# Kernel tuning notes

Measured on AMD Instinct MI355X. Metric: run time of the kernel, lower is better.

The kernel has to match this reference:

```python
import jax, jax.numpy as jnp
import numpy as np


def setup_inputs() -> dict:
    key = jax.random.key(0)
    k1, k2 = jax.random.split(key)
    B, S, D, L = 4, 4096, 256, 8921
    x = jax.random.normal(k1, (B, S, D), dtype=jnp.float32)
    U = jax.random.normal(k2, (L, D), dtype=jnp.float32)
    return {"x": x, "U": U}


def reference(x, U):
    # scores: [B, L, S] = U [L,D] @ x^T [B,D,S]
    scores = jnp.einsum('ld,bsd->bls', U, x)
    # softmax over seq dim (dim=2 in torch)
    alpha = jax.nn.softmax(scores, axis=2)
    # pooled: [B, L, D]
    out = jnp.einsum('bls,bsd->bld', alpha, x)
    return (out, alpha)
```

## Files before the change

kernel.cpp:

```cpp
#include <hip/hip_runtime.h>

#define B_DIM 4
#define S_DIM 4096
#define D_DIM 256
#define L_DIM 8921
#define L_PAD 8960

typedef _Float16 f16x8 __attribute__((ext_vector_type(8)));
typedef _Float16 f16x4 __attribute__((ext_vector_type(4)));
typedef float    f32x4 __attribute__((ext_vector_type(4)));

__device__ __forceinline__ void cp16(_Float16* lds, const _Float16* g) {
  __builtin_amdgcn_global_load_lds(
      (const __attribute__((address_space(1))) unsigned int*)g,
      (__attribute__((address_space(3))) unsigned int*)lds, 16, 0, 0);
}

__global__ __launch_bounds__(256) void k_split_x(const float* __restrict__ x,
                                                 _Float16* __restrict__ xh,
                                                 _Float16* __restrict__ xl) {
  const size_t i = ((size_t)blockIdx.x * 256 + threadIdx.x) * 4;
  float4 v = *(const float4*)(x + i);
  f16x4 h, l;
  h.x = (_Float16)v.x; l.x = (_Float16)(v.x - (float)h.x);
  h.y = (_Float16)v.y; l.y = (_Float16)(v.y - (float)h.y);
  h.z = (_Float16)v.z; l.z = (_Float16)(v.z - (float)h.z);
  h.w = (_Float16)v.w; l.w = (_Float16)(v.w - (float)h.w);
  *(f16x4*)(xh + i) = h;
  *(f16x4*)(xl + i) = l;
}

__global__ __launch_bounds__(256) void k_split_u(const float* __restrict__ U,
                                                 _Float16* __restrict__ uh,
                                                 _Float16* __restrict__ ul) {
  const size_t i = ((size_t)blockIdx.x * 256 + threadIdx.x) * 4;
  if (i >= (size_t)L_PAD * D_DIM) return;
  float4 v = make_float4(0.f, 0.f, 0.f, 0.f);
  if (i < (size_t)L_DIM * D_DIM) v = *(const float4*)(U + i);
  f16x4 h, l;
  h.x = (_Float16)v.x; l.x = (_Float16)(v.x - (float)h.x);
  h.y = (_Float16)v.y; l.y = (_Float16)(v.y - (float)h.y);
  h.z = (_Float16)v.z; l.z = (_Float16)(v.z - (float)h.z);
  h.w = (_Float16)v.w; l.w = (_Float16)(v.w - (float)h.w);
  *(f16x4*)(uh + i) = h;
  *(f16x4*)(ul + i) = l;
}

__global__ __launch_bounds__(256) void k_transpose(const float* __restrict__ x,
                                                   _Float16* __restrict__ xT) {
  __shared__ _Float16 t[32][33];
  const int s0 = blockIdx.x * 32, d0 = blockIdx.y * 32, b = blockIdx.z;
  const float* xb = x + (size_t)b * S_DIM * D_DIM;
  const int r = threadIdx.x >> 5, c = threadIdx.x & 31;
#pragma unroll
  for (int p = 0; p < 4; ++p) {
    const int row = r + p * 8;
    t[row][c] = (_Float16)xb[(size_t)(s0 + row) * D_DIM + d0 + c];
  }
  __syncthreads();
  _Float16* xtb = xT + (size_t)b * D_DIM * S_DIM;
#pragma unroll
  for (int p = 0; p < 4; ++p) {
    const int row = r + p * 8;
    xtb[(size_t)(d0 + row) * S_DIM + s0 + c] = t[c][row];
  }
}

__global__ __launch_bounds__(256) void k_scores(const _Float16* __restrict__ Uh,
                                                const _Float16* __restrict__ Ul,
                                                const _Float16* __restrict__ Xh,
                                                const _Float16* __restrict__ Xl,
                                                float* __restrict__ scores,
                                                float2* __restrict__ part) {
  const int s0 = blockIdx.x * 128;
  const int l0 = blockIdx.y * 128;
  const int b  = blockIdx.z;

  __shared__ __attribute__((aligned(16))) _Float16 Ah[128 * 32];
  __shared__ __attribute__((aligned(16))) _Float16 Al[128 * 32];
  __shared__ __attribute__((aligned(16))) _Float16 Bh[128 * 32];
  __shared__ __attribute__((aligned(16))) _Float16 Bl[128 * 32];

  const int tid = threadIdx.x;
  const int wave = tid >> 6, lane = tid & 63;
  const int wm = wave & 1, wn = wave >> 1;

  const _Float16* Xbh = Xh + (size_t)b * S_DIM * D_DIM;
  const _Float16* Xbl = Xl + (size_t)b * S_DIM * D_DIM;

  const int srow = tid >> 2;
  const int csrc = ((tid & 3) ^ ((tid >> 3) & 3)) * 8;
  const size_t urow0 = (size_t)(l0 + srow) * D_DIM + csrc;
  const size_t urow1 = urow0 + (size_t)64 * D_DIM;
  const size_t xrow0 = (size_t)(s0 + srow) * D_DIM + csrc;
  const size_t xrow1 = xrow0 + (size_t)64 * D_DIM;
  _Float16* d0 = (_Float16*)0 + tid * 8;
  const int ldso = tid * 8;

  const int frow = lane & 15;
  const int ck = ((lane >> 4) ^ ((frow >> 1) & 3)) * 8;

  f32x4 acc[4][4] = {};

  for (int k0 = 0; k0 < D_DIM; k0 += 32) {
    cp16(Ah + ldso,        Uh + urow0 + k0);
    cp16(Ah + 2048 + ldso, Uh + urow1 + k0);
    cp16(Al + ldso,        Ul + urow0 + k0);
    cp16(Al + 2048 + ldso, Ul + urow1 + k0);
    cp16(Bh + ldso,        Xbh + xrow0 + k0);
    cp16(Bh + 2048 + ldso, Xbh + xrow1 + k0);
    cp16(Bl + ldso,        Xbl + xrow0 + k0);
    cp16(Bl + 2048 + ldso, Xbl + xrow1 + k0);
    __syncthreads();

    f16x8 ah[4], al[4], bh[4], bl[4];
#pragma unroll
    for (int i = 0; i < 4; ++i) {
      const int ra = (wm * 64 + i * 16 + frow) * 32 + ck;
      const int rb = (wn * 64 + i * 16 + frow) * 32 + ck;
      ah[i] = *(const f16x8*)(Ah + ra);
      al[i] = *(const f16x8*)(Al + ra);
      bh[i] = *(const f16x8*)(Bh + rb);
      bl[i] = *(const f16x8*)(Bl + rb);
    }
#pragma unroll
    for (int i = 0; i < 4; ++i)
#pragma unroll
      for (int j = 0; j < 4; ++j) {
        acc[i][j] = __builtin_amdgcn_mfma_f32_16x16x32_f16(ah[i], bh[j], acc[i][j], 0, 0, 0);
        acc[i][j] = __builtin_amdgcn_mfma_f32_16x16x32_f16(ah[i], bl[j], acc[i][j], 0, 0, 0);
        acc[i][j] = __builtin_amdgcn_mfma_f32_16x16x32_f16(al[i], bh[j], acc[i][j], 0, 0, 0);
      }
    __syncthreads();
  }
  (void)d0;

  float* sc = scores + (size_t)b * L_DIM * S_DIM;
  const int hi = lane >> 4;
#pragma unroll
  for (int i = 0; i < 4; ++i)
#pragma unroll
    for (int j = 0; j < 4; ++j) {
      const int col = s0 + wn * 64 + j * 16 + (lane & 15);
#pragma unroll
      for (int r = 0; r < 4; ++r) {
        const int row = l0 + wm * 64 + i * 16 + hi * 4 + r;
        if (row < L_DIM) sc[(size_t)row * S_DIM + col] = acc[i][j][r];
      }
    }

  float* redm = (float*)Ah;
  float* reds = redm + 256;
#pragma unroll
  for (int i = 0; i < 4; ++i)
#pragma unroll
    for (int r = 0; r < 4; ++r) {
      float m = fmaxf(fmaxf(acc[i][0][r], acc[i][1][r]),
                      fmaxf(acc[i][2][r], acc[i][3][r]));
      m = fmaxf(m, __shfl_xor(m, 1));
      m = fmaxf(m, __shfl_xor(m, 2));
      m = fmaxf(m, __shfl_xor(m, 4));
      m = fmaxf(m, __shfl_xor(m, 8));
      float s = __expf(acc[i][0][r] - m) + __expf(acc[i][1][r] - m) +
                __expf(acc[i][2][r] - m) + __expf(acc[i][3][r] - m);
      s += __shfl_xor(s, 1);
      s += __shfl_xor(s, 2);
      s += __shfl_xor(s, 4);
      s += __shfl_xor(s, 8);
      if ((lane & 15) == 0) {
        const int row64 = i * 16 + hi * 4 + r;
        redm[(wm * 2 + wn) * 64 + row64] = m;
        reds[(wm * 2 + wn) * 64 + row64] = s;
      }
    }
  __syncthreads();
  if (tid < 128) {
    const int wmm = tid >> 6, r64 = tid & 63;
    const float m0 = redm[(wmm * 2 + 0) * 64 + r64];
    const float m1 = redm[(wmm * 2 + 1) * 64 + r64];
    const float s0v = reds[(wmm * 2 + 0) * 64 + r64];
    const float s1v = reds[(wmm * 2 + 1) * 64 + r64];
    const float m = fmaxf(m0, m1);
    const float s = s0v * __expf(m0 - m) + s1v * __expf(m1 - m);
    const int l = l0 + tid;
    if (l < L_DIM)
      part[((size_t)blockIdx.x * B_DIM + b) * L_PAD + l] = make_float2(m, s);
  }
}

__global__ __launch_bounds__(256) void k_sreduce(const float2* __restrict__ part,
                                                 float* __restrict__ stats) {
  const int idx = blockIdx.x * 256 + threadIdx.x;
  if (idx >= B_DIM * L_DIM) return;
  const int b = idx / L_DIM;
  const int l = idx - b * L_DIM;
  float2 v[32];
#pragma unroll
  for (int t = 0; t < 32; ++t) v[t] = part[((size_t)t * B_DIM + b) * L_PAD + l];
  float m = v[0].x;
#pragma unroll
  for (int t = 1; t < 32; ++t) m = fmaxf(m, v[t].x);
  float s = 0.f;
#pragma unroll
  for (int t = 0; t < 32; ++t) s += v[t].y * __expf(v[t].x - m);
  stats[2 * (size_t)idx]     = m;
  stats[2 * (size_t)idx + 1] = 1.0f / s;
}

__global__ __launch_bounds__(256) void k_out(const _Float16* __restrict__ XT,
                                             const float* __restrict__ stats,
                                             float* __restrict__ alpha,
                                             float* __restrict__ out) {
  const int l0 = blockIdx.x * 32;
  const int b  = blockIdx.y;
  const int tid = threadIdx.x;
  const int wave = tid >> 6, lane = tid & 63;

  __shared__ __attribute__((aligned(16))) _Float16 Aa[32 * 40];
  __shared__ __attribute__((aligned(16))) _Float16 Bb[256 * 40];
  __shared__ float sm[32], sr[32];

  if (tid < 32) {
    const int l = l0 + tid;
    float m = 0.f, r = 0.f;
    if (l < L_DIM) {
      const float* st = stats + ((size_t)b * L_DIM + l) * 2;
      m = st[0];
      r = st[1];
    }
    sm[tid] = m;
    sr[tid] = r;
  }
  __syncthreads();

  f32x4 acc[2][4] = {};
  float* al_base = alpha + (size_t)b * L_DIM * S_DIM;
  const _Float16* xt = XT + (size_t)b * D_DIM * S_DIM;

  const int arow = tid >> 3, aoff = (tid & 7) * 4;
  const int brow = tid >> 2, boff = (tid & 3) * 8;
  const float m_r = sm[arow], r_r = sr[arow];
  const int l_a = l0 + arow;
  const int frow = lane & 15, fk = (lane >> 4) * 8;

  for (int s0 = 0; s0 < S_DIM; s0 += 32) {
    float4 v = make_float4(0.f, 0.f, 0.f, 0.f);
    if (l_a < L_DIM) {
      float* ap = al_base + (size_t)l_a * S_DIM + s0 + aoff;
      v = *(const float4*)ap;
      v.x = __expf(v.x - m_r) * r_r;
      v.y = __expf(v.y - m_r) * r_r;
      v.z = __expf(v.z - m_r) * r_r;
      v.w = __expf(v.w - m_r) * r_r;
      *(float4*)ap = v;
    }
    f16x4 pk;
    pk.x = (_Float16)v.x;
    pk.y = (_Float16)v.y;
    pk.z = (_Float16)v.z;
    pk.w = (_Float16)v.w;
    *(f16x4*)(Aa + arow * 40 + aoff) = pk;
#pragma unroll
    for (int p = 0; p < 4; ++p) {
      const int row = brow + p * 64;
      *(uint4*)(Bb + row * 40 + boff) =
          *(const uint4*)(xt + (size_t)row * S_DIM + s0 + boff);
    }
    __syncthreads();

    f16x8 af[2], bf[4];
    af[0] = *(const f16x8*)(Aa + frow * 40 + fk);
    af[1] = *(const f16x8*)(Aa + (16 + frow) * 40 + fk);
#pragma unroll
    for (int j = 0; j < 4; ++j)
      bf[j] = *(const f16x8*)(Bb + (wave * 64 + j * 16 + frow) * 40 + fk);
#pragma unroll
    for (int i = 0; i < 2; ++i)
#pragma unroll
      for (int j = 0; j < 4; ++j)
        acc[i][j] = __builtin_amdgcn_mfma_f32_16x16x32_f16(af[i], bf[j], acc[i][j], 0, 0, 0);
    __syncthreads();
  }

  float* ob = out + (size_t)b * L_DIM * D_DIM;
#pragma unroll
  for (int i = 0; i < 2; ++i)
#pragma unroll
    for (int j = 0; j < 4; ++j) {
      const int d = wave * 64 + j * 16 + (lane & 15);
#pragma unroll
      for (int r = 0; r < 4; ++r) {
        const int l = l0 + i * 16 + (lane >> 4) * 4 + r;
        if (l < L_DIM) ob[(size_t)l * D_DIM + d] = acc[i][j][r];
      }
    }
}

extern "C" void kernel_launch(void* const* d_in, const int* in_sizes, int n_in,
                              void* d_out, int out_size, void* d_ws, size_t ws_size,
                              hipStream_t stream) {
  const float* x = (const float*)d_in[0];
  const float* U = (const float*)d_in[1];
  float* out   = (float*)d_out;
  float* alpha = out + (size_t)B_DIM * L_DIM * D_DIM;

  const size_t NX  = (size_t)B_DIM * S_DIM * D_DIM;
  const size_t NUP = (size_t)L_PAD * D_DIM;

  char* w = (char*)d_ws;
  _Float16* xh = (_Float16*)w; w += NX * 2;
  _Float16* xl = (_Float16*)w; w += NX * 2;
  _Float16* xT = (_Float16*)w; w += NX * 2;
  _Float16* uh = (_Float16*)w; w += NUP * 2;
  _Float16* ul = (_Float16*)w; w += NUP * 2;
  float* stats = (float*)w;    w += (size_t)B_DIM * L_DIM * 2 * sizeof(float);
  float2* part = (float2*)w;

  k_split_x<<<dim3((unsigned)(NX / 1024)), 256, 0, stream>>>(x, xh, xl);
  k_split_u<<<dim3((unsigned)(NUP / 1024)), 256, 0, stream>>>(U, uh, ul);
  k_transpose<<<dim3(S_DIM / 32, D_DIM / 32, B_DIM), 256, 0, stream>>>(x, xT);
  k_scores<<<dim3(S_DIM / 128, L_PAD / 128, B_DIM), 256, 0, stream>>>(
      uh, ul, xh, xl, alpha, part);
  k_sreduce<<<dim3((B_DIM * L_DIM + 255) / 256), 256, 0, stream>>>(part, stats);
  k_out<<<dim3((L_DIM + 31) / 32, B_DIM), 256, 0, stream>>>(xT, stats, alpha, out);
}
```

Before: 1.323 ms.

## Double-buffer k_out tiles with async LDS loads and prefetch of alpha

Rewrites the k_out main loop to double-buffer the A (softmax probabilities) and B (transposed x) tiles in LDS. The next X^T tile is issued via global_load_lds and the next alpha vector is prefetched into registers while the current tile's MFMAs run, and the trailing barrier is dropped. It also replaces the padded LDS layout with an XOR-swizzled one. The aim is to hide global load latency and cut one barrier per iteration, at the cost of doubled LDS use and a more delicate ordering of barriers around the buffers.

```diff
diff --git a/kernel.cpp b/kernel.cpp
--- a/kernel.cpp
+++ b/kernel.cpp
@@ -94,7 +94,6 @@
   const size_t urow1 = urow0 + (size_t)64 * D_DIM;
   const size_t xrow0 = (size_t)(s0 + srow) * D_DIM + csrc;
   const size_t xrow1 = xrow0 + (size_t)64 * D_DIM;
-  _Float16* d0 = (_Float16*)0 + tid * 8;
   const int ldso = tid * 8;
 
   const int frow = lane & 15;
@@ -133,7 +132,6 @@
       }
     __syncthreads();
   }
-  (void)d0;
 
   float* sc = scores + (size_t)b * L_DIM * S_DIM;
   const int hi = lane >> 4;
@@ -216,8 +214,8 @@
   const int tid = threadIdx.x;
   const int wave = tid >> 6, lane = tid & 63;
 
-  __shared__ __attribute__((aligned(16))) _Float16 Aa[32 * 40];
-  __shared__ __attribute__((aligned(16))) _Float16 Bb[256 * 40];
+  __shared__ __attribute__((aligned(16))) _Float16 Aa[2][32 * 32];
+  __shared__ __attribute__((aligned(16))) _Float16 Bb[2][256 * 32];
   __shared__ float sm[32], sr[32];
 
   if (tid < 32) {
@@ -237,49 +235,64 @@
   float* al_base = alpha + (size_t)b * L_DIM * S_DIM;
   const _Float16* xt = XT + (size_t)b * D_DIM * S_DIM;
 
-  const int arow = tid >> 3, aoff = (tid & 7) * 4;
-  const int brow = tid >> 2, boff = (tid & 3) * 8;
+  const int arow = tid >> 3, a8 = tid & 7;
+  const int aoff = a8 * 4;
   const float m_r = sm[arow], r_r = sr[arow];
   const int l_a = l0 + arow;
-  const int frow = lane & 15, fk = (lane >> 4) * 8;
-
-  for (int s0 = 0; s0 < S_DIM; s0 += 32) {
-    float4 v = make_float4(0.f, 0.f, 0.f, 0.f);
-    if (l_a < L_DIM) {
-      float* ap = al_base + (size_t)l_a * S_DIM + s0 + aoff;
-      v = *(const float4*)ap;
-      v.x = __expf(v.x - m_r) * r_r;
-      v.y = __expf(v.y - m_r) * r_r;
-      v.z = __expf(v.z - m_r) * r_r;
-      v.w = __expf(v.w - m_r) * r_r;
-      *(float4*)ap = v;
-    }
+  const int aphys = arow * 32 + (((a8 >> 1) ^ ((arow >> 1) & 3)) * 8) + (a8 & 1) * 4;
+
+  const int brow = tid >> 2;
+  const int bsrc = ((tid & 3) ^ ((tid >> 3) & 3)) * 8;
+  const int bdst = tid * 8;
+
+  const int frow = lane & 15;
+  const int ck = ((lane >> 4) ^ ((frow >> 1) & 3)) * 8;
+
+  float* ap0 = (l_a < L_DIM) ? (al_base + (size_t)l_a * S_DIM + aoff) : nullptr;
+
+#pragma unroll
+  for (int p = 0; p < 4; ++p)
+    cp16(&Bb[0][p * 2048 + bdst], xt + (size_t)(brow + p * 64) * S_DIM + bsrc);
+  float4 va = make_float4(0.f, 0.f, 0.f, 0.f);
+  if (ap0) va = *(const float4*)ap0;
+
+  const int NT = S_DIM / 32;
+  for (int t = 0; t < NT; ++t) {
+    const int cur = t & 1;
+    float4 e;
+    e.x = __expf(va.x - m_r) * r_r;
+    e.y = __expf(va.y - m_r) * r_r;
+    e.z = __expf(va.z - m_r) * r_r;
+    e.w = __expf(va.w - m_r) * r_r;
     f16x4 pk;
-    pk.x = (_Float16)v.x;
-    pk.y = (_Float16)v.y;
-    pk.z = (_Float16)v.z;
-    pk.w = (_Float16)v.w;
-    *(f16x4*)(Aa + arow * 40 + aoff) = pk;
-#pragma unroll
-    for (int p = 0; p < 4; ++p) {
-      const int row = brow + p * 64;
-      *(uint4*)(Bb + row * 40 + boff) =
-          *(const uint4*)(xt + (size_t)row * S_DIM + s0 + boff);
-    }
+    pk.x = (_Float16)e.x;
+    pk.y = (_Float16)e.y;
+    pk.z = (_Float16)e.z;
+    pk.w = (_Float16)e.w;
+    *(f16x4*)(&Aa[cur][aphys]) = pk;
     __syncthreads();
 
-    f16x8 af[2], bf[4];
-    af[0] = *(const f16x8*)(Aa + frow * 40 + fk);
-    af[1] = *(const f16x8*)(Aa + (16 + frow) * 40 + fk);
+    if (ap0) *(float4*)(ap0 + (size_t)t * 32) = e;
+    if (t + 1 < NT) {
+      const int s1 = (t + 1) * 32;
+#pragma unroll
+      for (int p = 0; p < 4; ++p)
+        cp16(&Bb[cur ^ 1][p * 2048 + bdst],
+             xt + (size_t)(brow + p * 64) * S_DIM + s1 + bsrc);
+      if (ap0) va = *(const float4*)(ap0 + (size_t)(t + 1) * 32);
+    }
+
+    f16x8 af0 = *(const f16x8*)(&Aa[cur][frow * 32 + ck]);
+    f16x8 af1 = *(const f16x8*)(&Aa[cur][(16 + frow) * 32 + ck]);
+    f16x8 bf[4];
 #pragma unroll
     for (int j = 0; j < 4; ++j)
-      bf[j] = *(const f16x8*)(Bb + (wave * 64 + j * 16 + frow) * 40 + fk);
-#pragma unroll
-    for (int i = 0; i < 2; ++i)
-#pragma unroll
-      for (int j = 0; j < 4; ++j)
-        acc[i][j] = __builtin_amdgcn_mfma_f32_16x16x32_f16(af[i], bf[j], acc[i][j], 0, 0, 0);
-    __syncthreads();
+      bf[j] = *(const f16x8*)(&Bb[cur][(wave * 64 + j * 16 + frow) * 32 + ck]);
+#pragma unroll
+    for (int j = 0; j < 4; ++j) {
+      acc[0][j] = __builtin_amdgcn_mfma_f32_16x16x32_f16(af0, bf[j], acc[0][j], 0, 0, 0);
+      acc[1][j] = __builtin_amdgcn_mfma_f32_16x16x32_f16(af1, bf[j], acc[1][j], 0, 0, 0);
+    }
   }
 
   float* ob = out + (size_t)b * L_DIM * D_DIM;
```

Result: slower. 1.370 ms (+3.5%).

## Double-buffer score GEMM and split alpha normalization out of output GEMM

Applied to the files above, without the earlier changes.

The score kernel now uses two LDS buffers so the async global-to-LDS copies for the next K chunk overlap with the current chunk's MFMA work, and one barrier per iteration is removed. Softmax normalization of alpha moves into its own elementwise kernel. The output GEMM then reads normalized alpha, uses a larger 64-row tile with a 64-wide K step and XOR-swizzled LDS, and loads xT through async LDS copies. The split costs an extra read and write pass over the large alpha array, in exchange for a simpler, better-reused output GEMM. Doubling the score kernel's LDS may lower occupancy.

```diff
diff --git a/kernel.cpp b/kernel.cpp
--- a/kernel.cpp
+++ b/kernel.cpp
@@ -76,10 +76,10 @@
   const int l0 = blockIdx.y * 128;
   const int b  = blockIdx.z;
 
-  __shared__ __attribute__((aligned(16))) _Float16 Ah[128 * 32];
-  __shared__ __attribute__((aligned(16))) _Float16 Al[128 * 32];
-  __shared__ __attribute__((aligned(16))) _Float16 Bh[128 * 32];
-  __shared__ __attribute__((aligned(16))) _Float16 Bl[128 * 32];
+  __shared__ __attribute__((aligned(16))) _Float16 Ah[2][128 * 32];
+  __shared__ __attribute__((aligned(16))) _Float16 Al[2][128 * 32];
+  __shared__ __attribute__((aligned(16))) _Float16 Bh[2][128 * 32];
+  __shared__ __attribute__((aligned(16))) _Float16 Bl[2][128 * 32];
 
   const int tid = threadIdx.x;
   const int wave = tid >> 6, lane = tid & 63;
@@ -94,7 +94,6 @@
   const size_t urow1 = urow0 + (size_t)64 * D_DIM;
   const size_t xrow0 = (size_t)(s0 + srow) * D_DIM + csrc;
   const size_t xrow1 = xrow0 + (size_t)64 * D_DIM;
-  _Float16* d0 = (_Float16*)0 + tid * 8;
   const int ldso = tid * 8;
 
   const int frow = lane & 15;
@@ -102,26 +101,34 @@
 
   f32x4 acc[4][4] = {};
 
-  for (int k0 = 0; k0 < D_DIM; k0 += 32) {
-    cp16(Ah + ldso,        Uh + urow0 + k0);
-    cp16(Ah + 2048 + ldso, Uh + urow1 + k0);
-    cp16(Al + ldso,        Ul + urow0 + k0);
-    cp16(Al + 2048 + ldso, Ul + urow1 + k0);
-    cp16(Bh + ldso,        Xbh + xrow0 + k0);
-    cp16(Bh + 2048 + ldso, Xbh + xrow1 + k0);
-    cp16(Bl + ldso,        Xbl + xrow0 + k0);
-    cp16(Bl + 2048 + ldso, Xbl + xrow1 + k0);
+  auto stage = [&](int nb, int k0) {
+    cp16(&Ah[nb][ldso],        Uh + urow0 + k0);
+    cp16(&Ah[nb][2048 + ldso], Uh + urow1 + k0);
+    cp16(&Al[nb][ldso],        Ul + urow0 + k0);
+    cp16(&Al[nb][2048 + ldso], Ul + urow1 + k0);
+    cp16(&Bh[nb][ldso],        Xbh + xrow0 + k0);
+    cp16(&Bh[nb][2048 + ldso], Xbh + xrow1 + k0);
+    cp16(&Bl[nb][ldso],        Xbl + xrow0 + k0);
+    cp16(&Bl[nb][2048 + ldso], Xbl + xrow1 + k0);
+  };
+
+  stage(0, 0);
+
+  const int NK = D_DIM / 32;
+  for (int ks = 0; ks < NK; ++ks) {
+    const int cur = ks & 1;
     __syncthreads();
+    if (ks + 1 < NK) stage(cur ^ 1, (ks + 1) * 32);
 
     f16x8 ah[4], al[4], bh[4], bl[4];
 #pragma unroll
     for (int i = 0; i < 4; ++i) {
       const int ra = (wm * 64 + i * 16 + frow) * 32 + ck;
       const int rb = (wn * 64 + i * 16 + frow) * 32 + ck;
-      ah[i] = *(const f16x8*)(Ah + ra);
-      al[i] = *(const f16x8*)(Al + ra);
-      bh[i] = *(const f16x8*)(Bh + rb);
-      bl[i] = *(const f16x8*)(Bl + rb);
+      ah[i] = *(const f16x8*)(&Ah[cur][ra]);
+      al[i] = *(const f16x8*)(&Al[cur][ra]);
+      bh[i] = *(const f16x8*)(&Bh[cur][rb]);
+      bl[i] = *(const f16x8*)(&Bl[cur][rb]);
     }
 #pragma unroll
     for (int i = 0; i < 4; ++i)
@@ -131,9 +138,7 @@
         acc[i][j] = __builtin_amdgcn_mfma_f32_16x16x32_f16(ah[i], bl[j], acc[i][j], 0, 0, 0);
         acc[i][j] = __builtin_amdgcn_mfma_f32_16x16x32_f16(al[i], bh[j], acc[i][j], 0, 0, 0);
       }
-    __syncthreads();
-  }
-  (void)d0;
+  }
 
   float* sc = scores + (size_t)b * L_DIM * S_DIM;
   const int hi = lane >> 4;
@@ -149,7 +154,7 @@
       }
     }
 
-  float* redm = (float*)Ah;
+  float* redm = (float*)&Ah[0][0];
   float* reds = redm + 256;
 #pragma unroll
   for (int i = 0; i < 4; ++i)
@@ -207,84 +212,100 @@
   stats[2 * (size_t)idx + 1] = 1.0f / s;
 }
 
+__global__ __launch_bounds__(256) void k_alpha(const float* __restrict__ stats,
+                                               float* __restrict__ alpha) {
+  const int l = blockIdx.y, b = blockIdx.z;
+  const float* st = stats + ((size_t)b * L_DIM + l) * 2;
+  const float m = st[0], r = st[1];
+  float4* p = (float4*)(alpha + ((size_t)b * L_DIM + l) * S_DIM) +
+              blockIdx.x * 256 + threadIdx.x;
+  float4 v = *p;
+  v.x = __expf(v.x - m) * r;
+  v.y = __expf(v.y - m) * r;
+  v.z = __expf(v.z - m) * r;
+  v.w = __expf(v.w - m) * r;
+  *p = v;
+}
+
 __global__ __launch_bounds__(256) void k_out(const _Float16* __restrict__ XT,
-                                             const float* __restrict__ stats,
-                                             float* __restrict__ alpha,
+                                             const float* __restrict__ alpha,
                                              float* __restrict__ out) {
-  const int l0 = blockIdx.x * 32;
+  const int l0 = blockIdx.x * 64;
   const int b  = blockIdx.y;
   const int tid = threadIdx.x;
   const int wave = tid >> 6, lane = tid & 63;
 
-  __shared__ __attribute__((aligned(16))) _Float16 Aa[32 * 40];
-  __shared__ __attribute__((aligned(16))) _Float16 Bb[256 * 40];
-  __shared__ float sm[32], sr[32];
-
-  if (tid < 32) {
-    const int l = l0 + tid;
-    float m = 0.f, r = 0.f;
-    if (l < L_DIM) {
-      const float* st = stats + ((size_t)b * L_DIM + l) * 2;
-      m = st[0];
-      r = st[1];
-    }
-    sm[tid] = m;
-    sr[tid] = r;
-  }
-  __syncthreads();
-
-  f32x4 acc[2][4] = {};
-  float* al_base = alpha + (size_t)b * L_DIM * S_DIM;
+  __shared__ __attribute__((aligned(16))) _Float16 Aa[64 * 64];
+  __shared__ __attribute__((aligned(16))) _Float16 Bb[256 * 64];
+
   const _Float16* xt = XT + (size_t)b * D_DIM * S_DIM;
-
-  const int arow = tid >> 3, aoff = (tid & 7) * 4;
-  const int brow = tid >> 2, boff = (tid & 3) * 8;
-  const float m_r = sm[arow], r_r = sr[arow];
-  const int l_a = l0 + arow;
-  const int frow = lane & 15, fk = (lane >> 4) * 8;
-
-  for (int s0 = 0; s0 < S_DIM; s0 += 32) {
-    float4 v = make_float4(0.f, 0.f, 0.f, 0.f);
-    if (l_a < L_DIM) {
-      float* ap = al_base + (size_t)l_a * S_DIM + s0 + aoff;
-      v = *(const float4*)ap;
-      v.x = __expf(v.x - m_r) * r_r;
-      v.y = __expf(v.y - m_r) * r_r;
-      v.z = __expf(v.z - m_r) * r_r;
-      v.w = __expf(v.w - m_r) * r_r;
-      *(float4*)ap = v;
-    }
-    f16x4 pk;
-    pk.x = (_Float16)v.x;
-    pk.y = (_Float16)v.y;
-    pk.z = (_Float16)v.z;
-    pk.w = (_Float16)v.w;
-    *(f16x4*)(Aa + arow * 40 + aoff) = pk;
-#pragma unroll
-    for (int p = 0; p < 4; ++p) {
-      const int row = brow + p * 64;
-      *(uint4*)(Bb + row * 40 + boff) =
-          *(const uint4*)(xt + (size_t)row * S_DIM + s0 + boff);
-    }
+  const float* al = alpha + (size_t)b * L_DIM * S_DIM;
+
+  const int ar  = tid >> 2;
+  const int ac0 = (tid & 3) * 2;
+  const int l_a = l0 + ar;
+  const bool amask = l_a < L_DIM;
+  const float* arow = al + (size_t)l_a * S_DIM;
+  const int apx0 = ar * 64 + ((ac0)     ^ (ar & 7)) * 8;
+  const int apx1 = ar * 64 + ((ac0 + 1) ^ (ar & 7)) * 8;
+
+  const int br   = tid >> 3;
+  const int bsrc = ((tid & 7) ^ (br & 7)) * 8;
+  const int bdst = tid * 8;
+
+  const int frow = lane & 15, hi = lane >> 4;
+
+  f32x4 acc[4][4] = {};
+
+  for (int ks = 0; ks < S_DIM / 64; ++ks) {
+    const int s0 = ks * 64;
+#pragma unroll
+    for (int p = 0; p < 8; ++p)
+      cp16(Bb + p * 2048 + bdst,
+           xt + (size_t)(br + p * 32) * S_DIM + s0 + bsrc);
+    float4 v0 = make_float4(0.f, 0.f, 0.f, 0.f), v1 = v0, v2 = v0, v3 = v0;
+    if (amask) {
+      const float* ap = arow + s0 + ac0 * 8;
+      v0 = *(const float4*)(ap);
+      v1 = *(const float4*)(ap + 4);
+      v2 = *(const float4*)(ap + 8);
+      v3 = *(const float4*)(ap + 12);
+    }
+    f16x8 w0, w1;
+    w0[0] = (_Float16)v0.x; w0[1] = (_Float16)v0.y;
+    w0[2] = (_Float16)v0.z; w0[3] = (_Float16)v0.w;
+    w0[4] = (_Float16)v1.x; w0[5] = (_Float16)v1.y;
+    w0[6] = (_Float16)v1.z; w0[7] = (_Float16)v1.w;
+    w1[0] = (_Float16)v2.x; w1[1] = (_Float16)v2.y;
+    w1[2] = (_Float16)v2.z; w1[3] = (_Float16)v2.w;
+    w1[4] = (_Float16)v3.x; w1[5] = (_Float16)v3.y;
+    w1[6] = (_Float16)v3.z; w1[7] = (_Float16)v3.w;
+    *(f16x8*)(Aa + apx0) = w0;
+    *(f16x8*)(Aa + apx1) = w1;
     __syncthreads();
 
-    f16x8 af[2], bf[4];
-    af[0] = *(const f16x8*)(Aa + frow * 40 + fk);
-    af[1] = *(const f16x8*)(Aa + (16 + frow) * 40 + fk);
-#pragma unroll
-    for (int j = 0; j < 4; ++j)
-      bf[j] = *(const f16x8*)(Bb + (wave * 64 + j * 16 + frow) * 40 + fk);
-#pragma unroll
-    for (int i = 0; i < 2; ++i)
+#pragma unroll
+    for (int kh = 0; kh < 2; ++kh) {
+      const int pck = ((kh * 4 + hi) ^ (frow & 7)) * 8;
+      f16x8 af[4], bf[4];
+#pragma unroll
+      for (int i = 0; i < 4; ++i)
+        af[i] = *(const f16x8*)(Aa + (i * 16 + frow) * 64 + pck);
 #pragma unroll
       for (int j = 0; j < 4; ++j)
-        acc[i][j] = __builtin_amdgcn_mfma_f32_16x16x32_f16(af[i], bf[j], acc[i][j], 0, 0, 0);
+        bf[j] = *(const f16x8*)(Bb + (wave * 64 + j * 16 + frow) * 64 + pck);
+#pragma unroll
+      for (int i = 0; i < 4; ++i)
+#pragma unroll
+        for (int j = 0; j < 4; ++j)
+          acc[i][j] = __builtin_amdgcn_mfma_f32_16x16x32_f16(af[i], bf[j], acc[i][j], 0, 0, 0);
+    }
     __syncthreads();
   }
 
   float* ob = out + (size_t)b * L_DIM * D_DIM;
 #pragma unroll
-  for (int i = 0; i < 2; ++i)
+  for (int i = 0; i < 4; ++i)
 #pragma unroll
     for (int j = 0; j < 4; ++j) {
       const int d = wave * 64 + j * 16 + (lane & 15);
@@ -322,5 +343,6 @@
   k_scores<<<dim3(S_DIM / 128, L_PAD / 128, B_DIM), 256, 0, stream>>>(
       uh, ul, xh, xl, alpha, part);
   k_sreduce<<<dim3((B_DIM * L_DIM + 255) / 256), 256, 0, stream>>>(part, stats);
-  k_out<<<dim3((L_DIM + 31) / 32, B_DIM), 256, 0, stream>>>(xT, stats, alpha, out);
-}
+  k_alpha<<<dim3(S_DIM / 1024, L_DIM, B_DIM), 256, 0, stream>>>(stats, alpha);
+  k_out<<<dim3((L_DIM + 63) / 64, B_DIM), 256, 0, stream>>>(xT, alpha, out);
+}
```

Result: faster. 1.254 ms (-5.2%).
